# Kernel optimization log

Hardware: AMD Instinct MI355X
Metric: run time of the kernel (lower is better)

The kernel has to match this reference:

```python
import jax, jax.numpy as jnp
import numpy as np

N_HEADS = 16
HEAD_DIM = 64
D_MODEL = N_HEADS * HEAD_DIM
MASK_NUM = -2.0**32 + 1.0
LN_EPS = 1e-8


def setup_inputs() -> dict:
    key = jax.random.key(0)
    ks = jax.random.split(key, 6)
    B, S = 2, 2048
    queries = jax.random.normal(ks[0], (B, S, D_MODEL), dtype=jnp.float32)
    keys = jax.random.normal(ks[1], (B, S, D_MODEL), dtype=jnp.float32)
    values = jax.random.normal(ks[2], (B, S, D_MODEL), dtype=jnp.float32)
    lim = np.sqrt(6.0 / (D_MODEL + D_MODEL)).astype(np.float32)  # glorot_uniform
    Wq = jax.random.uniform(ks[3], (D_MODEL, D_MODEL), jnp.float32, -lim, lim)
    Wk = jax.random.uniform(ks[4], (D_MODEL, D_MODEL), jnp.float32, -lim, lim)
    Wv = jax.random.uniform(ks[5], (D_MODEL, D_MODEL), jnp.float32, -lim, lim)
    gamma = jnp.ones((D_MODEL,), jnp.float32)
    beta = jnp.zeros((D_MODEL,), jnp.float32)
    return {"queries": queries, "keys": keys, "values": values,
            "Wq": Wq, "Wk": Wk, "Wv": Wv, "gamma": gamma, "beta": beta}


def _split_heads(x):
    # [B, S, H*dh] -> tf.split(axis=2)+concat(axis=0) order: [H*B, S, dh]
    B, S, _ = x.shape
    return x.reshape(B, S, N_HEADS, HEAD_DIM).transpose(2, 0, 1, 3).reshape(N_HEADS * B, S, HEAD_DIM)


def _merge_heads(x, B):
    # [H*B, S, dh] -> [B, S, H*dh]
    S = x.shape[1]
    return x.reshape(N_HEADS, B, S, HEAD_DIM).transpose(1, 2, 0, 3).reshape(B, S, D_MODEL)


def reference(queries, keys, values, Wq, Wk, Wv, gamma, beta):
    B = queries.shape[0]
    q = _split_heads(queries @ Wq)   # [HB, Sq, dh]
    k = _split_heads(keys @ Wk)      # [HB, Sk, dh]
    v = _split_heads(values @ Wv)    # [HB, Sk, dh]

    scores = jnp.einsum('bqd,bkd->bqk', q, k) / jnp.float32(np.sqrt(HEAD_DIM))
    # key padding mask: positions whose projected key is all-zero
    kmask = jnp.sign(jnp.sum(jnp.abs(k), axis=-1))  # [HB, Sk]
    scores = jnp.where(kmask[:, None, :] == 0, jnp.float32(MASK_NUM), scores)
    attn = jax.nn.softmax(scores, axis=-1)
    # query mask: zero out rows whose projected query is all-zero
    qmask = jnp.sign(jnp.sum(jnp.abs(q), axis=-1))  # [HB, Sq]
    attn = attn * qmask[:, :, None]
    att_out = jnp.einsum('bqk,bkd->bqd', attn, v)   # [HB, Sq, dh]
    att_out = _merge_heads(att_out, B)               # [B, Sq, D]

    x = att_out + queries
    mean = jnp.mean(x, axis=-1, keepdims=True)
    var = jnp.mean((x - mean) ** 2, axis=-1, keepdims=True)
    norm = (x - mean) / jnp.sqrt(var + LN_EPS)
    return gamma * norm + beta
```

## Files before the change

kernel.cpp:

```cpp
#include <hip/hip_runtime.h>

#define DM   1024
#define SEQ  2048
#define NH   16
#define HD   64
#define ROWS 4096

typedef unsigned short u16;
typedef unsigned int   u32;
typedef __attribute__((ext_vector_type(8))) __bf16 bf16x8;
typedef __attribute__((ext_vector_type(4))) float  f32x4;
typedef __attribute__((ext_vector_type(16))) float f32x16;

__device__ __forceinline__ u16 f2bf(float f) {
  u32 u = __builtin_bit_cast(u32, f);
  u += 0x7fffu + ((u >> 16) & 1u);
  return (u16)(u >> 16);
}

__device__ __forceinline__ void async16(const void* g, void* lds) {
  __builtin_amdgcn_global_load_lds((const __attribute__((address_space(1))) u32*)g,
                                   (__attribute__((address_space(3))) u32*)lds, 16, 0, 0);
}


__global__ __launch_bounds__(256) void k_cvt_act(const float* __restrict__ q,
                                                 const float* __restrict__ k,
                                                 const float* __restrict__ v,
                                                 u16* __restrict__ dst) {
  const float* src = blockIdx.z == 0 ? q : (blockIdx.z == 1 ? k : v);
  u16* d = dst + (size_t)blockIdx.z * ((size_t)ROWS * DM);
  size_t i = ((size_t)blockIdx.x * 256 + threadIdx.x) * 8;
  float4 a = *(const float4*)(src + i);
  float4 b = *(const float4*)(src + i + 4);
  u32 w0 = (u32)f2bf(a.x) | ((u32)f2bf(a.y) << 16);
  u32 w1 = (u32)f2bf(a.z) | ((u32)f2bf(a.w) << 16);
  u32 w2 = (u32)f2bf(b.x) | ((u32)f2bf(b.y) << 16);
  u32 w3 = (u32)f2bf(b.z) | ((u32)f2bf(b.w) << 16);
  uint4 o4; o4.x = w0; o4.y = w1; o4.z = w2; o4.w = w3;
  *(uint4*)(d + i) = o4;
}

__global__ __launch_bounds__(256) void k_cvt_wt(const float* __restrict__ Wq,
                                                const float* __restrict__ Wk,
                                                const float* __restrict__ Wv,
                                                u16* __restrict__ wt) {
  __shared__ float t[32][33];
  const float* W = blockIdx.z == 0 ? Wq : (blockIdx.z == 1 ? Wk : Wv);
  u16* D = wt + (size_t)blockIdx.z * (DM * DM);
  int bx = blockIdx.x * 32, by = blockIdx.y * 32;
  int x = threadIdx.x, y = threadIdx.y;
  for (int i = 0; i < 32; i += 8) t[y + i][x] = W[(size_t)(by + y + i) * DM + bx + x];
  __syncthreads();
  for (int i = 0; i < 32; i += 8) D[(size_t)(bx + y + i) * DM + by + x] = f2bf(t[x][y + i]);
}


__global__ __launch_bounds__(256) void k_gemm(const u16* __restrict__ Abase,
                                              const u16* __restrict__ Btbase,
                                              u16* __restrict__ Cbase) {
  __shared__ u16 As[128 * 64];
  __shared__ u16 Bs[128 * 64];
  const int z = blockIdx.z;
  const u16* A  = Abase  + (size_t)z * ((size_t)ROWS * DM);
  const u16* Bt = Btbase + (size_t)z * (DM * DM);
  u16* C        = Cbase  + (size_t)z * ((size_t)ROWS * DM);
  const float sc = (z == 0) ? 0.18033688011112043f : 1.0f;
  int tid = threadIdx.x, w = tid >> 6, l = tid & 63;
  int fr = l & 15, fq = l >> 4;
  int bid = blockIdx.y * 8 + blockIdx.x;
  int nb  = (bid & 7) * 32 + (bid >> 3);
  int m0 = (nb >> 3) * 128, n0 = (nb & 7) * 128;
  int wr = (w >> 1) * 64, wc = (w & 1) * 64;
  f32x4 acc[4][4];
  for (int i = 0; i < 4; ++i) for (int j = 0; j < 4; ++j) acc[i][j] = (f32x4){0.f, 0.f, 0.f, 0.f};

  for (int k0 = 0; k0 < DM; k0 += 64) {
    __syncthreads();
    for (int c = 0; c < 4; ++c) {
      int loff = (c * 4 + w) * 1024;
      int eoff = (loff >> 1) + l * 8;
      int row = eoff >> 6;
      int blk = (eoff & 63) >> 3;
      int gblk = blk ^ (row & 7);
      async16(A  + (size_t)(m0 + row) * DM + k0 + (gblk << 3), (char*)As + loff);
      async16(Bt + (size_t)(n0 + row) * DM + k0 + (gblk << 3), (char*)Bs + loff);
    }
    __syncthreads();
    for (int ks = 0; ks < 2; ++ks) {
      bf16x8 af[4], bf[4];
      for (int i = 0; i < 4; ++i) {
        int row = wr + i * 16 + fr;
        af[i] = *(const bf16x8*)(As + row * 64 + (((ks * 4 + fq) ^ (row & 7)) << 3));
      }
      for (int j = 0; j < 4; ++j) {
        int row = wc + j * 16 + fr;
        bf[j] = *(const bf16x8*)(Bs + row * 64 + (((ks * 4 + fq) ^ (row & 7)) << 3));
      }
      for (int i = 0; i < 4; ++i)
        for (int j = 0; j < 4; ++j)
          acc[i][j] = __builtin_amdgcn_mfma_f32_16x16x32_bf16(af[i], bf[j], acc[i][j], 0, 0, 0);
    }
  }
  for (int i = 0; i < 4; ++i)
    for (int j = 0; j < 4; ++j)
      for (int jj = 0; jj < 4; ++jj) {
        int row = m0 + wr + i * 16 + fq * 4 + jj;
        int col = n0 + wc + j * 16 + fr;
        C[(size_t)row * DM + col] = f2bf(acc[i][j][jj] * sc);
      }
}


__global__ __launch_bounds__(256) void k_vt(const u16* __restrict__ vproj,
                                            u16* __restrict__ vt) {
  __shared__ u16 t[64][64];
  int y = blockIdx.y;
  int h = y >> 1, b = y & 1;
  int s0 = blockIdx.x * 64;
  int tid = threadIdx.x;
  for (int c = 0; c < 2; ++c) {
    int rr = c * 32 + (tid >> 3);
    int blk = tid & 7;
    uint4 vv = *(const uint4*)(vproj + (size_t)(b * SEQ + s0 + rr) * DM + h * 64 + blk * 8);
    *(uint4*)(&t[rr][((blk ^ (rr & 7)) * 8)]) = vv;
  }
  __syncthreads();
  for (int c = 0; c < 2; ++c) {
    int d = c * 32 + (tid >> 3);
    int p = tid & 7;
    int B = p ^ (d & 7);
    int g = B >> 1, half = B & 1;
    u16 tmp[8];
    for (int j = 0; j < 8; ++j) {
      int kj = (j < 4) ? (4 * half + j) : (8 + 4 * half + (j - 4));
      int ss = 16 * g + kj;
      tmp[j] = t[ss][((d >> 3) ^ (ss & 7)) * 8 + (d & 7)];
    }
    *(uint4*)(vt + (size_t)(y * 64 + d) * SEQ + s0 + p * 8) = *(uint4*)tmp;
  }
}


__global__ __launch_bounds__(256, 4) void k_attn(const u16* __restrict__ Qp,
                                                 const u16* __restrict__ Kp,
                                                 const u16* __restrict__ Vt,
                                                 float* __restrict__ att) {
  __shared__ u16 lds[20480];
  const int tid = threadIdx.x, w = tid >> 6, l = tid & 63;
  const int lrow = l & 31, h = l >> 5;
  const int qh = w & 1, kh = w >> 1;
  const int g = blockIdx.x;
  const int vy = (g & 7) * 4 + ((g >> 3) & 3);
  const int vx = g >> 5;
  const int head = vy >> 1, b = vy & 1;
  const int hcol = head * 64;
  const int q0w = vx * 64 + qh * 32;

  const u16* qrow = Qp + (size_t)(b * SEQ + q0w + lrow) * DM + hcol + h * 8;
  bf16x8 qb0 = *(const bf16x8*)(qrow);
  bf16x8 qb1 = *(const bf16x8*)(qrow + 16);
  bf16x8 qb2 = *(const bf16x8*)(qrow + 32);
  bf16x8 qb3 = *(const bf16x8*)(qrow + 48);

  const int sw = lrow & 7;
  const int kbase = kh * 4096 + lrow * 128;
  const int B0 = kbase + (((0 + h) ^ sw) << 4);
  const int B1 = kbase + (((2 + h) ^ sw) << 4);
  const int B2 = kbase + (((4 + h) ^ sw) << 4);
  const int B3 = kbase + (((6 + h) ^ sw) << 4);

  const int vfb = lrow * 128;
  const int V0 = vfb + (((4 * kh + 0 + h) ^ sw) << 4);
  const int V1 = vfb + (((4 * kh + 2 + h) ^ sw) << 4);

  const int ldo0 = w * 1024, ldo1 = (4 + w) * 1024;
  const int e0 = (ldo0 >> 1) + l * 8, e1 = (ldo1 >> 1) + l * 8;
  const int r0 = e0 >> 6, r1 = e1 >> 6;
  const int kb0 = ((e0 & 63) >> 3) ^ (r0 & 7), kb1 = ((e1 & 63) >> 3) ^ (r1 & 7);
  const u32 koff0 = (u32)((b * SEQ + r0) * DM + hcol + kb0 * 8);
  const u32 koff1 = (u32)((b * SEQ + r1) * DM + hcol + kb1 * 8);
  const u32 voff0 = (u32)((vy * 64 + r0) * SEQ + (e0 & 63));
  const u32 voff1 = (u32)((vy * 64 + r1) * SEQ + (e1 & 63));

  const f32x16 kzero = {};
  f32x16 ot0 = {}, ot1 = {};
  float lacc = 0.f;
  bf16x8 pbP0 = {}, pbP1 = {};

  {
    char* base = (char*)lds;
    async16(Kp + koff0, base + ldo0);
    async16(Kp + koff1, base + ldo1);
    async16(Vt + voff0, base + 16384 + ldo0);
    async16(Vt + voff1, base + 16384 + ldo1);
  }
  __syncthreads();

  int vprev = 16384, vcur = 0, vnxt = 8192;
  for (int t = 0; t < SEQ / 64; ++t) {
    char* base = (char*)lds;
    if (t < SEQ / 64 - 1) {
      u32 kadv = (u32)(t + 1) * (64 * DM);
      u32 vadv = (u32)(t + 1) * 64;
      char* kd = base + ((t + 1) & 1) * 8192;
      char* vd = base + 16384 + vnxt;
      async16(Kp + kadv + koff0, kd + ldo0);
      async16(Kp + kadv + koff1, kd + ldo1);
      async16(Vt + vadv + voff0, vd + ldo0);
      async16(Vt + vadv + voff1, vd + ldo1);
    }

    const char* Kb = base + (t & 1) * 8192;
    bf16x8 a0 = *(const bf16x8*)(Kb + B0);
    bf16x8 a1 = *(const bf16x8*)(Kb + B1);
    bf16x8 a2 = *(const bf16x8*)(Kb + B2);
    bf16x8 a3 = *(const bf16x8*)(Kb + B3);
    __builtin_amdgcn_s_setprio(1);
    f32x16 st = __builtin_amdgcn_mfma_f32_32x32x16_bf16(a0, qb0, kzero, 0, 0, 0);
    st = __builtin_amdgcn_mfma_f32_32x32x16_bf16(a1, qb1, st, 0, 0, 0);
    st = __builtin_amdgcn_mfma_f32_32x32x16_bf16(a2, qb2, st, 0, 0, 0);
    st = __builtin_amdgcn_mfma_f32_32x32x16_bf16(a3, qb3, st, 0, 0, 0);
    __builtin_amdgcn_s_setprio(0);

    if (t) {
      const char* Vb = base + 16384 + vprev;
      bf16x8 vf0 = *(const bf16x8*)(Vb + V0);
      bf16x8 vf1 = *(const bf16x8*)(Vb + V1);
      bf16x8 vf2 = *(const bf16x8*)(Vb + 4096 + V0);
      bf16x8 vf3 = *(const bf16x8*)(Vb + 4096 + V1);
      __builtin_amdgcn_s_setprio(1);
      ot0 = __builtin_amdgcn_mfma_f32_32x32x16_bf16(vf0, pbP0, ot0, 0, 0, 0);
      ot0 = __builtin_amdgcn_mfma_f32_32x32x16_bf16(vf1, pbP1, ot0, 0, 0, 0);
      ot1 = __builtin_amdgcn_mfma_f32_32x32x16_bf16(vf2, pbP0, ot1, 0, 0, 0);
      ot1 = __builtin_amdgcn_mfma_f32_32x32x16_bf16(vf3, pbP1, ot1, 0, 0, 0);
      __builtin_amdgcn_s_setprio(0);
    }

    f32x16 p;
#pragma unroll
    for (int i = 0; i < 16; ++i) p[i] = __builtin_amdgcn_exp2f(st[i]);
    float s0 = (p[0] + p[1]) + (p[2] + p[3]);
    float s1 = (p[4] + p[5]) + (p[6] + p[7]);
    float s2 = (p[8] + p[9]) + (p[10] + p[11]);
    float s3 = (p[12] + p[13]) + (p[14] + p[15]);
    lacc += (s0 + s1) + (s2 + s3);
#pragma unroll
    for (int j = 0; j < 8; ++j) {
      pbP0[j] = (__bf16)p[j];
      pbP1[j] = (__bf16)p[8 + j];
    }

    __syncthreads();
    int tmp = vprev; vprev = vcur; vcur = vnxt; vnxt = tmp;
  }

  {
    const char* Vb = (const char*)lds + 16384 + vprev;
    bf16x8 vf0 = *(const bf16x8*)(Vb + V0);
    bf16x8 vf1 = *(const bf16x8*)(Vb + V1);
    bf16x8 vf2 = *(const bf16x8*)(Vb + 4096 + V0);
    bf16x8 vf3 = *(const bf16x8*)(Vb + 4096 + V1);
    ot0 = __builtin_amdgcn_mfma_f32_32x32x16_bf16(vf0, pbP0, ot0, 0, 0, 0);
    ot0 = __builtin_amdgcn_mfma_f32_32x32x16_bf16(vf1, pbP1, ot0, 0, 0, 0);
    ot1 = __builtin_amdgcn_mfma_f32_32x32x16_bf16(vf2, pbP0, ot1, 0, 0, 0);
    ot1 = __builtin_amdgcn_mfma_f32_32x32x16_bf16(vf3, pbP1, ot1, 0, 0, 0);
  }
  lacc += __shfl_xor(lacc, 32);

  float* mrg = (float*)lds;
  const int slot = qh * 2176;
  if (kh) {
#pragma unroll
    for (int r = 0; r < 16; ++r) {
      mrg[slot + r * 64 + l] = ot0[r];
      mrg[slot + (16 + r) * 64 + l] = ot1[r];
    }
    mrg[slot + 2048 + l] = lacc;
  }
  __syncthreads();
  if (!kh) {
    float inv = 1.f / (lacc + mrg[slot + 2048 + l]);
    float* orow = att + (size_t)(b * SEQ + q0w + lrow) * DM + hcol + 4 * h;
#pragma unroll
    for (int G = 0; G < 4; ++G) {
      float4 w0;
      w0.x = (ot0[4 * G + 0] + mrg[slot + (4 * G + 0) * 64 + l]) * inv;
      w0.y = (ot0[4 * G + 1] + mrg[slot + (4 * G + 1) * 64 + l]) * inv;
      w0.z = (ot0[4 * G + 2] + mrg[slot + (4 * G + 2) * 64 + l]) * inv;
      w0.w = (ot0[4 * G + 3] + mrg[slot + (4 * G + 3) * 64 + l]) * inv;
      *(float4*)(orow + 8 * G) = w0;
      float4 w1;
      w1.x = (ot1[4 * G + 0] + mrg[slot + (16 + 4 * G + 0) * 64 + l]) * inv;
      w1.y = (ot1[4 * G + 1] + mrg[slot + (16 + 4 * G + 1) * 64 + l]) * inv;
      w1.z = (ot1[4 * G + 2] + mrg[slot + (16 + 4 * G + 2) * 64 + l]) * inv;
      w1.w = (ot1[4 * G + 3] + mrg[slot + (16 + 4 * G + 3) * 64 + l]) * inv;
      *(float4*)(orow + 32 + 8 * G) = w1;
    }
  }
}


__global__ __launch_bounds__(256) void k_ln(const float* __restrict__ att,
                                            const float* __restrict__ qin,
                                            const float* __restrict__ gamma,
                                            const float* __restrict__ beta,
                                            float* __restrict__ out) {
  __shared__ float rsum[4], rsum2[4];
  int row = blockIdx.x, t = threadIdx.x;
  size_t off = (size_t)row * DM + t * 4;
  float4 a = *(const float4*)(att + off);
  float4 q = *(const float4*)(qin + off);
  float4 x; x.x = a.x + q.x; x.y = a.y + q.y; x.z = a.z + q.z; x.w = a.w + q.w;
  float s = x.x + x.y + x.z + x.w;
  float s2 = x.x * x.x + x.y * x.y + x.z * x.z + x.w * x.w;
  for (int o2 = 1; o2 < 64; o2 <<= 1) { s += __shfl_xor(s, o2); s2 += __shfl_xor(s2, o2); }
  int w = t >> 6, l = t & 63;
  if (l == 0) { rsum[w] = s; rsum2[w] = s2; }
  __syncthreads();
  s = rsum[0] + rsum[1] + rsum[2] + rsum[3];
  s2 = rsum2[0] + rsum2[1] + rsum2[2] + rsum2[3];
  float mean = s * (1.f / DM);
  float var = s2 * (1.f / DM) - mean * mean;
  float rstd = rsqrtf(var + 1e-8f);
  float4 g = *(const float4*)(gamma + t * 4);
  float4 be = *(const float4*)(beta + t * 4);
  float4 r;
  r.x = (x.x - mean) * rstd * g.x + be.x;
  r.y = (x.y - mean) * rstd * g.y + be.y;
  r.z = (x.z - mean) * rstd * g.z + be.z;
  r.w = (x.w - mean) * rstd * g.w + be.w;
  *(float4*)(out + off) = r;
}


extern "C" void kernel_launch(void* const* d_in, const int* in_sizes, int n_in,
                              void* d_out, int out_size, void* d_ws, size_t ws_size,
                              hipStream_t stream) {
  (void)in_sizes; (void)n_in; (void)out_size; (void)ws_size;
  const float* q     = (const float*)d_in[0];
  const float* k     = (const float*)d_in[1];
  const float* v     = (const float*)d_in[2];
  const float* Wq    = (const float*)d_in[3];
  const float* Wk    = (const float*)d_in[4];
  const float* Wv    = (const float*)d_in[5];
  const float* gamma = (const float*)d_in[6];
  const float* beta  = (const float*)d_in[7];
  float* out = (float*)d_out;
  char* ws = (char*)d_ws;

  const size_t ACT_B = 3ull * ROWS * DM * 2;
  const size_t WT_B  = 3ull * DM * DM * 2;

  u16* actb  = (u16*)ws;
  u16* wtb   = (u16*)(ws + ACT_B);
  u16* projb = (u16*)(ws + ACT_B + WT_B);
  u16* vt    = (u16*)ws;
  float* att = (float*)(ws + 8ull * 1024 * 1024);

  k_cvt_act<<<dim3(2048, 1, 3), 256, 0, stream>>>(q, k, v, actb);
  k_cvt_wt<<<dim3(32, 32, 3), dim3(32, 8), 0, stream>>>(Wq, Wk, Wv, wtb);
  k_gemm<<<dim3(8, 32, 3), 256, 0, stream>>>(actb, wtb, projb);
  k_vt<<<dim3(SEQ / 64, NH * 2), 256, 0, stream>>>(projb + 2ull * ROWS * DM, vt);
  k_attn<<<1024, 256, 0, stream>>>(projb, projb + (size_t)ROWS * DM, vt, att);
  k_ln<<<ROWS, 256, 0, stream>>>(att, q, gamma, beta, out);
}
```

Measured before the change: 119.7 us.

## Overlap attention K/V prefetch using partial vmcnt waits and shrink GEMM k-tile

The attention loop replaces __syncthreads (which waits for every outstanding load) with explicit s_waitcnt vmcnt(6) plus raw barriers. This lets the next tile's async K/V loads stay in flight while the current tile is computed. To keep the per-iteration load count constant, the final iteration issues a redundant clamped load. Separately, the projection GEMM k-step drops from 64 to 32 with a matching swizzle, halving LDS use at the cost of twice as many barriers per K sweep.

```diff
diff --git a/kernel.cpp b/kernel.cpp
--- a/kernel.cpp
+++ b/kernel.cpp
@@ -59,8 +59,8 @@
 __global__ __launch_bounds__(256) void k_gemm(const u16* __restrict__ Abase,
                                               const u16* __restrict__ Btbase,
                                               u16* __restrict__ Cbase) {
-  __shared__ u16 As[128 * 64];
-  __shared__ u16 Bs[128 * 64];
+  __shared__ u16 As[128 * 32];
+  __shared__ u16 Bs[128 * 32];
   const int z = blockIdx.z;
   const u16* A  = Abase  + (size_t)z * ((size_t)ROWS * DM);
   const u16* Bt = Btbase + (size_t)z * (DM * DM);
@@ -75,32 +75,30 @@
   f32x4 acc[4][4];
   for (int i = 0; i < 4; ++i) for (int j = 0; j < 4; ++j) acc[i][j] = (f32x4){0.f, 0.f, 0.f, 0.f};
 
-  for (int k0 = 0; k0 < DM; k0 += 64) {
+  for (int k0 = 0; k0 < DM; k0 += 32) {
     __syncthreads();
-    for (int c = 0; c < 4; ++c) {
+    for (int c = 0; c < 2; ++c) {
       int loff = (c * 4 + w) * 1024;
       int eoff = (loff >> 1) + l * 8;
-      int row = eoff >> 6;
-      int blk = (eoff & 63) >> 3;
-      int gblk = blk ^ (row & 7);
+      int row = eoff >> 5;
+      int blk = (eoff & 31) >> 3;
+      int gblk = blk ^ ((row >> 1) & 3);
       async16(A  + (size_t)(m0 + row) * DM + k0 + (gblk << 3), (char*)As + loff);
       async16(Bt + (size_t)(n0 + row) * DM + k0 + (gblk << 3), (char*)Bs + loff);
     }
     __syncthreads();
-    for (int ks = 0; ks < 2; ++ks) {
-      bf16x8 af[4], bf[4];
-      for (int i = 0; i < 4; ++i) {
-        int row = wr + i * 16 + fr;
-        af[i] = *(const bf16x8*)(As + row * 64 + (((ks * 4 + fq) ^ (row & 7)) << 3));
-      }
-      for (int j = 0; j < 4; ++j) {
-        int row = wc + j * 16 + fr;
-        bf[j] = *(const bf16x8*)(Bs + row * 64 + (((ks * 4 + fq) ^ (row & 7)) << 3));
-      }
-      for (int i = 0; i < 4; ++i)
-        for (int j = 0; j < 4; ++j)
-          acc[i][j] = __builtin_amdgcn_mfma_f32_16x16x32_bf16(af[i], bf[j], acc[i][j], 0, 0, 0);
-    }
+    bf16x8 af[4], bf[4];
+    for (int i = 0; i < 4; ++i) {
+      int row = wr + i * 16 + fr;
+      af[i] = *(const bf16x8*)(As + row * 32 + ((fq ^ ((row >> 1) & 3)) << 3));
+    }
+    for (int j = 0; j < 4; ++j) {
+      int row = wc + j * 16 + fr;
+      bf[j] = *(const bf16x8*)(Bs + row * 32 + ((fq ^ ((row >> 1) & 3)) << 3));
+    }
+    for (int i = 0; i < 4; ++i)
+      for (int j = 0; j < 4; ++j)
+        acc[i][j] = __builtin_amdgcn_mfma_f32_16x16x32_bf16(af[i], bf[j], acc[i][j], 0, 0, 0);
   }
   for (int i = 0; i < 4; ++i)
     for (int j = 0; j < 4; ++j)
@@ -188,28 +186,28 @@
   float lacc = 0.f;
   bf16x8 pbP0 = {}, pbP1 = {};
 
-  {
-    char* base = (char*)lds;
-    async16(Kp + koff0, base + ldo0);
-    async16(Kp + koff1, base + ldo1);
-    async16(Vt + voff0, base + 16384 + ldo0);
-    async16(Vt + voff1, base + 16384 + ldo1);
-  }
-  __syncthreads();
-
-  int vprev = 16384, vcur = 0, vnxt = 8192;
+  char* base = (char*)lds;
+  async16(Kp + koff0, base + ldo0);
+  async16(Kp + koff1, base + ldo1);
+  async16(Vt + voff0, base + 16384 + ldo0);
+  async16(Vt + voff1, base + 16384 + ldo1);
+
+  int vwr = 1, vcr = 0, vrd = 2;
   for (int t = 0; t < SEQ / 64; ++t) {
-    char* base = (char*)lds;
-    if (t < SEQ / 64 - 1) {
-      u32 kadv = (u32)(t + 1) * (64 * DM);
-      u32 vadv = (u32)(t + 1) * 64;
+    {
+      u32 u = (t + 1 < SEQ / 64) ? (u32)(t + 1) : (u32)(SEQ / 64 - 1);
+      u32 kadv = u * (64 * DM);
+      u32 vadv = u * 64;
       char* kd = base + ((t + 1) & 1) * 8192;
-      char* vd = base + 16384 + vnxt;
+      char* vd = base + 16384 + vwr * 8192;
       async16(Kp + kadv + koff0, kd + ldo0);
       async16(Kp + kadv + koff1, kd + ldo1);
       async16(Vt + vadv + voff0, vd + ldo0);
       async16(Vt + vadv + voff1, vd + ldo1);
     }
+    asm volatile("s_waitcnt vmcnt(6)" ::: "memory");
+    __builtin_amdgcn_s_barrier();
+    asm volatile("" ::: "memory");
 
     const char* Kb = base + (t & 1) * 8192;
     bf16x8 a0 = *(const bf16x8*)(Kb + B0);
@@ -224,7 +222,7 @@
     __builtin_amdgcn_s_setprio(0);
 
     if (t) {
-      const char* Vb = base + 16384 + vprev;
+      const char* Vb = base + 16384 + vrd * 8192;
       bf16x8 vf0 = *(const bf16x8*)(Vb + V0);
       bf16x8 vf1 = *(const bf16x8*)(Vb + V1);
       bf16x8 vf2 = *(const bf16x8*)(Vb + 4096 + V0);
@@ -251,12 +249,18 @@
       pbP1[j] = (__bf16)p[8 + j];
     }
 
-    __syncthreads();
-    int tmp = vprev; vprev = vcur; vcur = vnxt; vnxt = tmp;
-  }
-
+    asm volatile("" ::: "memory");
+    __builtin_amdgcn_s_barrier();
+    asm volatile("" ::: "memory");
+
+    int tmp = vrd; vrd = vcr; vcr = vwr; vwr = tmp;
+  }
+
+  asm volatile("s_waitcnt vmcnt(0)" ::: "memory");
+  __builtin_amdgcn_s_barrier();
+  asm volatile("" ::: "memory");
   {
-    const char* Vb = (const char*)lds + 16384 + vprev;
+    const char* Vb = base + 16384 + vrd * 8192;
     bf16x8 vf0 = *(const bf16x8*)(Vb + V0);
     bf16x8 vf1 = *(const bf16x8*)(Vb + V1);
     bf16x8 vf2 = *(const bf16x8*)(Vb + 4096 + V0);
@@ -268,6 +272,7 @@
   }
   lacc += __shfl_xor(lacc, 32);
 
+  __syncthreads();
   float* mrg = (float*)lds;
   const int slot = qh * 2176;
   if (kh) {
```

After: 114.7 us. -4.2%, faster.
